# Optimization experiments

Measured on AMD Instinct MI355X. Metric: run time of the kernel, lower is better.

Reference implementation:

```python
import jax, jax.numpy as jnp
import numpy as np

EMBED_DIM = 384


def setup_inputs() -> dict:
    key = jax.random.key(0)
    k1, k2, k3 = jax.random.split(key, 3)
    B, P, N, C = 32, 4, 1024, EMBED_DIM
    x = jax.random.normal(k1, (B, P, N, C), dtype=jnp.float32)
    # 1x1 Conv2D on channel-last == linear on last dim; kernel [Cin, Cout]
    w_qkv = jax.random.normal(k2, (C, 1 + 2 * C), dtype=jnp.float32) * (1.0 / np.sqrt(C))
    b_qkv = jnp.zeros((1 + 2 * C,), dtype=jnp.float32)
    w_proj = jax.random.normal(k3, (C, C), dtype=jnp.float32) * (1.0 / np.sqrt(C))
    b_proj = jnp.zeros((C,), dtype=jnp.float32)
    return {"x": x, "w_qkv": w_qkv, "b_qkv": b_qkv, "w_proj": w_proj, "b_proj": b_proj}


def reference(x, w_qkv, b_qkv, w_proj, b_proj):
    C = EMBED_DIM
    # qkv pointwise conv: [B,P,N,C] @ [C, 1+2C]
    qkv = jnp.einsum('bpnc,cd->bpnd', x, w_qkv) + b_qkv
    query = qkv[..., :1]                 # [B,P,N,1]
    key_t = qkv[..., 1:1 + C]            # [B,P,N,C]
    value = qkv[..., 1 + C:]             # [B,P,N,C]
    # NOTE: softmax over the trailing axis of size 1 (faithful to source) -> all ones
    context_scores = jax.nn.softmax(query, axis=-1)
    # key * scores, reduce-sum over patch-index axis (axis=2), keepdims
    context_vector = jnp.sum(key_t * context_scores, axis=2, keepdims=True)  # [B,P,1,C]
    gated = jax.nn.relu(value) * context_vector                              # [B,P,N,C]
    out = jnp.einsum('bpnc,cd->bpnd', gated, w_proj) + b_proj
    return out
```

## Files before the change

kernel.cpp:

```cpp
#include <hip/hip_runtime.h>
#include <hip/hip_bf16.h>
#include <type_traits>
#include <utility>

#define C_    384
#define N_    1024
#define G_    128
#define QKVD  769

typedef float  f32x4 __attribute__((ext_vector_type(4)));
typedef short  s16x8 __attribute__((ext_vector_type(8)));
typedef __bf16 b16x8 __attribute__((ext_vector_type(8)));

template <typename V, typename = void>
struct mfma_takes : std::false_type {};
template <typename V>
struct mfma_takes<V, std::void_t<decltype(__builtin_amdgcn_mfma_f32_16x16x32_bf16(
    std::declval<V>(), std::declval<V>(), std::declval<f32x4>(), 0, 0, 0))>>
    : std::true_type {};

using frag_t = std::conditional_t<mfma_takes<s16x8>::value, s16x8, b16x8>;

template <typename V>
__device__ __forceinline__ f32x4 mfma_bf16(V a, V b, f32x4 c) {
  return __builtin_amdgcn_mfma_f32_16x16x32_bf16(a, b, c, 0, 0, 0);
}

__device__ __forceinline__ unsigned short f2bf(float f) {
  union { float f; unsigned u; } v; v.f = f;
  unsigned r = v.u + 0x7fffu + ((v.u >> 16) & 1u);
  return (unsigned short)(r >> 16);
}
__device__ __forceinline__ unsigned pack2(float lo, float hi) {
  return (unsigned)f2bf(lo) | ((unsigned)f2bf(hi) << 16);
}

__global__ __launch_bounds__(384) void k_xsum(const float* __restrict__ x,
                                              float* __restrict__ xsum) {
  __shared__ float sh[4][C_];
  const int tid = threadIdx.x;
  const int c4  = (tid % 96) * 4;
  const int rg  = tid / 96;
  const int b   = blockIdx.x;
  const int g   = b >> 3;
  const float* p = x + ((size_t)b * 128 + (size_t)rg * 32) * C_ + c4;
  f32x4 s = {0.f, 0.f, 0.f, 0.f};
#pragma unroll 8
  for (int r = 0; r < 32; ++r) {
    float4 v = *(const float4*)(p + (size_t)r * C_);
    s.x += v.x; s.y += v.y; s.z += v.z; s.w += v.w;
  }
  *(f32x4*)&sh[rg][c4] = s;
  __syncthreads();
  if (rg == 0) {
#pragma unroll
    for (int j = 0; j < 4; ++j) {
      float v = sh[0][c4 + j] + sh[1][c4 + j] + sh[2][c4 + j] + sh[3][c4 + j];
      atomicAdd(&xsum[g * C_ + c4 + j], v);
    }
  }
}

__global__ void k_cv(const float* __restrict__ xsum, const float* __restrict__ w_qkv,
                     const float* __restrict__ b_qkv, float* __restrict__ cv) {
  __shared__ float xs[C_];
  int g = blockIdx.x, c = threadIdx.x;
  xs[c] = xsum[g * C_ + c];
  __syncthreads();
  float acc = 0.f;
#pragma unroll 4
  for (int k = 0; k < C_; ++k) acc += xs[k] * w_qkv[k * QKVD + 1 + c];
  cv[g * C_ + c] = acc + (float)N_ * b_qkv[1 + c];
}

__global__ void k_pack(const float* __restrict__ w_qkv, const float* __restrict__ w_proj,
                       unsigned short* __restrict__ pWv, unsigned short* __restrict__ pWp) {
  int bid = blockIdx.x;
  int mat = bid / 288;
  int r   = bid % 288;
  int kk = r / 24, nf = r % 24;
  int lane = threadIdx.x;
  int kbase = kk * 32 + (lane >> 4) * 8;
  int n = nf * 16 + (lane & 15);
  unsigned v[4];
#pragma unroll
  for (int jj = 0; jj < 4; ++jj) {
    int k0 = kbase + jj * 2;
    float f0 = mat ? w_proj[(size_t)k0 * C_ + n]       : w_qkv[(size_t)k0 * QKVD + 385 + n];
    float f1 = mat ? w_proj[(size_t)(k0 + 1) * C_ + n] : w_qkv[(size_t)(k0 + 1) * QKVD + 385 + n];
    v[jj] = (unsigned)f2bf(f0) | ((unsigned)f2bf(f1) << 16);
  }
  unsigned short* dst = (mat ? pWp : pWv) + ((size_t)r * 64 + lane) * 8;
  uint4 w; w.x = v[0]; w.y = v[1]; w.z = v[2]; w.w = v[3];
  *(uint4*)dst = w;
}

__global__ __launch_bounds__(512) void k_fused(
    const float* __restrict__ x, const unsigned short* __restrict__ pWv,
    const unsigned short* __restrict__ pWp, const float* __restrict__ cv,
    const float* __restrict__ b_qkv, const float* __restrict__ b_proj,
    float* __restrict__ out) {
  __shared__ __align__(16) char tile[32 * 768];
  __shared__ float cv_l[C_], bv_l[C_], bp_l[C_];

  const int tid  = threadIdx.x;
  const int lane = tid & 63;
  const int wv   = tid >> 6;
  const int R0   = blockIdx.x * 32;
  const int g    = R0 >> 10;

  if (tid < C_) {
    cv_l[tid] = cv[g * C_ + tid];
    bv_l[tid] = b_qkv[1 + C_ + tid];
    bp_l[tid] = b_proj[tid];
  }

  {
    const float* xg = x + (size_t)R0 * C_;
#pragma unroll
    for (int j = 0; j < 3; ++j) {
      int ch  = tid + j * 512;
      int row = ch / 48;
      int c8  = (ch % 48) * 8;
      const float4* s0 = (const float4*)(xg + (size_t)row * C_ + c8);
      float4 a = s0[0], b = s0[1];
      uint4 w;
      w.x = pack2(a.x, a.y); w.y = pack2(a.z, a.w);
      w.z = pack2(b.x, b.y); w.w = pack2(b.z, b.w);
      int byte = (row * 768 + c8 * 2) ^ ((row & 7) << 4);
      *(uint4*)(tile + byte) = w;
    }
  }
  __syncthreads();

  const f32x4 zero = {0.f, 0.f, 0.f, 0.f};
  f32x4 acc[2][3];
#pragma unroll
  for (int m = 0; m < 2; ++m)
#pragma unroll
    for (int n = 0; n < 3; ++n) acc[m][n] = zero;

  for (int kk = 0; kk < 12; ++kk) {
    frag_t A[2], Bv[3];
    int kb2 = (kk * 32 + (lane >> 4) * 8) * 2;
#pragma unroll
    for (int m = 0; m < 2; ++m) {
      int row = m * 16 + (lane & 15);
      A[m] = *(const frag_t*)(tile + ((row * 768 + kb2) ^ ((row & 7) << 4)));
    }
    const unsigned short* bp_ = pWv + ((size_t)(kk * 24 + wv * 3) * 64 + lane) * 8;
#pragma unroll
    for (int n = 0; n < 3; ++n) Bv[n] = *(const frag_t*)(bp_ + (size_t)n * 64 * 8);
#pragma unroll
    for (int m = 0; m < 2; ++m)
#pragma unroll
      for (int n = 0; n < 3; ++n) acc[m][n] = mfma_bf16(A[m], Bv[n], acc[m][n]);
  }
  __syncthreads();

#pragma unroll
  for (int m = 0; m < 2; ++m) {
#pragma unroll
    for (int n = 0; n < 3; ++n) {
      int col = wv * 48 + n * 16 + (lane & 15);
      float cvv = cv_l[col], bvv = bv_l[col];
#pragma unroll
      for (int r = 0; r < 4; ++r) {
        int row = m * 16 + (lane >> 4) * 4 + r;
        float val = fmaxf(acc[m][n][r] + bvv, 0.f) * cvv;
        *(unsigned short*)(tile + ((row * 768 + col * 2) ^ ((row & 7) << 4))) = f2bf(val);
      }
    }
  }
  __syncthreads();

#pragma unroll
  for (int m = 0; m < 2; ++m)
#pragma unroll
    for (int n = 0; n < 3; ++n) acc[m][n] = zero;

  for (int kk = 0; kk < 12; ++kk) {
    frag_t A[2], Bv[3];
    int kb2 = (kk * 32 + (lane >> 4) * 8) * 2;
#pragma unroll
    for (int m = 0; m < 2; ++m) {
      int row = m * 16 + (lane & 15);
      A[m] = *(const frag_t*)(tile + ((row * 768 + kb2) ^ ((row & 7) << 4)));
    }
    const unsigned short* bp_ = pWp + ((size_t)(kk * 24 + wv * 3) * 64 + lane) * 8;
#pragma unroll
    for (int n = 0; n < 3; ++n) Bv[n] = *(const frag_t*)(bp_ + (size_t)n * 64 * 8);
#pragma unroll
    for (int m = 0; m < 2; ++m)
#pragma unroll
      for (int n = 0; n < 3; ++n) acc[m][n] = mfma_bf16(A[m], Bv[n], acc[m][n]);
  }

#pragma unroll
  for (int m = 0; m < 2; ++m) {
#pragma unroll
    for (int n = 0; n < 3; ++n) {
      int col = wv * 48 + n * 16 + (lane & 15);
      float bpv = bp_l[col];
#pragma unroll
      for (int r = 0; r < 4; ++r) {
        int row = m * 16 + (lane >> 4) * 4 + r;
        out[(size_t)(R0 + row) * C_ + col] = acc[m][n][r] + bpv;
      }
    }
  }
}

extern "C" void kernel_launch(void* const* d_in, const int* in_sizes, int n_in,
                              void* d_out, int out_size, void* d_ws, size_t ws_size,
                              hipStream_t stream) {
  const float* x      = (const float*)d_in[0];
  const float* w_qkv  = (const float*)d_in[1];
  const float* b_qkv  = (const float*)d_in[2];
  const float* w_proj = (const float*)d_in[3];
  const float* b_proj = (const float*)d_in[4];
  float* out = (float*)d_out;

  float* xsum = (float*)d_ws;
  float* cvp  = xsum + G_ * C_;
  unsigned short* pWv = (unsigned short*)(cvp + G_ * C_);
  unsigned short* pWp = pWv + C_ * C_;

  hipMemsetAsync(xsum, 0, G_ * C_ * sizeof(float), stream);
  k_xsum<<<1024, 384, 0, stream>>>(x, xsum);
  k_pack<<<576, 64, 0, stream>>>(w_qkv, w_proj, pWv, pWp);
  k_cv<<<G_, C_, 0, stream>>>(xsum, w_qkv, b_qkv, cvp);
  k_fused<<<4096, 512, 0, stream>>>(x, pWv, pWp, cvp, b_qkv, b_proj, out);
}
```

Before: 234.3 us.

## Pre-convert x to swizzled bf16 tiles while summing, stage via global_load_lds

A new prep kernel reads x once, computes the per-group column sums, and writes a bf16 copy of x already laid out in the swizzled LDS tile format into workspace. The fused kernel then copies each tile straight into LDS with global_load_lds instead of reading fp32 x and converting it, so the second full fp32 read of x becomes a half-size bf16 read. The cost is an extra write and read of the bf16 image in global memory. The new path runs only when the workspace is large enough; otherwise the old path is kept.

```diff
diff --git a/kernel.cpp b/kernel.cpp
--- a/kernel.cpp
+++ b/kernel.cpp
@@ -3,10 +3,11 @@
 #include <type_traits>
 #include <utility>
 
-#define C_    384
-#define N_    1024
-#define G_    128
-#define QKVD  769
+#define C_     384
+#define N_     1024
+#define G_     128
+#define QKVD   769
+#define TILE_B 24576
 
 typedef float  f32x4 __attribute__((ext_vector_type(4)));
 typedef short  s16x8 __attribute__((ext_vector_type(8)));
@@ -33,6 +34,53 @@
 }
 __device__ __forceinline__ unsigned pack2(float lo, float hi) {
   return (unsigned)f2bf(lo) | ((unsigned)f2bf(hi) << 16);
+}
+
+__device__ __forceinline__ void stage16(const char* g, char* lbase, int lane) {
+#if __has_builtin(__builtin_amdgcn_global_load_lds)
+  __builtin_amdgcn_global_load_lds(
+      (const __attribute__((address_space(1))) void*)g,
+      (__attribute__((address_space(3))) void*)lbase, 16, 0, 0);
+#else
+  *(uint4*)(lbase + lane * 16) = *(const uint4*)g;
+#endif
+}
+
+__global__ __launch_bounds__(384) void k_prep(const float* __restrict__ x,
+                                              char* __restrict__ xbb,
+                                              float* __restrict__ xsum) {
+  __shared__ float csum[C_];
+  const int b    = blockIdx.x;
+  const int g    = b >> 4;
+  const int tid  = threadIdx.x;
+  const int col8 = (tid % 48) * 8;
+  const int rg   = tid / 48;
+  csum[tid] = 0.f;
+  __syncthreads();
+
+  const float* xg = x + ((size_t)b * 64 + (size_t)rg * 8) * C_ + col8;
+  char* img = xbb + (size_t)b * 2 * TILE_B;
+  float s0=0,s1=0,s2=0,s3=0,s4=0,s5=0,s6=0,s7=0;
+#pragma unroll
+  for (int j = 0; j < 8; ++j) {
+    int row = rg * 8 + j;
+    float4 a = *(const float4*)(xg + (size_t)j * C_);
+    float4 c = *(const float4*)(xg + (size_t)j * C_ + 4);
+    uint4 w;
+    w.x = pack2(a.x, a.y); w.y = pack2(a.z, a.w);
+    w.z = pack2(c.x, c.y); w.w = pack2(c.z, c.w);
+    int rt = row & 31;
+    int tl = row >> 5;
+    *(uint4*)(img + tl * TILE_B + ((rt * 768 + col8 * 2) ^ ((rt & 7) << 4))) = w;
+    s0 += a.x; s1 += a.y; s2 += a.z; s3 += a.w;
+    s4 += c.x; s5 += c.y; s6 += c.z; s7 += c.w;
+  }
+  atomicAdd(&csum[col8 + 0], s0); atomicAdd(&csum[col8 + 1], s1);
+  atomicAdd(&csum[col8 + 2], s2); atomicAdd(&csum[col8 + 3], s3);
+  atomicAdd(&csum[col8 + 4], s4); atomicAdd(&csum[col8 + 5], s5);
+  atomicAdd(&csum[col8 + 6], s6); atomicAdd(&csum[col8 + 7], s7);
+  __syncthreads();
+  atomicAdd(&xsum[g * C_ + tid], csum[tid]);
 }
 
 __global__ __launch_bounds__(384) void k_xsum(const float* __restrict__ x,
@@ -95,11 +143,12 @@
   *(uint4*)dst = w;
 }
 
+template <bool PRE>
 __global__ __launch_bounds__(512) void k_fused(
-    const float* __restrict__ x, const unsigned short* __restrict__ pWv,
-    const unsigned short* __restrict__ pWp, const float* __restrict__ cv,
-    const float* __restrict__ b_qkv, const float* __restrict__ b_proj,
-    float* __restrict__ out) {
+    const float* __restrict__ x, const char* __restrict__ xbb,
+    const unsigned short* __restrict__ pWv, const unsigned short* __restrict__ pWp,
+    const float* __restrict__ cv, const float* __restrict__ b_qkv,
+    const float* __restrict__ b_proj, float* __restrict__ out) {
   __shared__ __align__(16) char tile[32 * 768];
   __shared__ float cv_l[C_], bv_l[C_], bp_l[C_];
 
@@ -115,7 +164,14 @@
     bp_l[tid] = b_proj[tid];
   }
 
-  {
+  if constexpr (PRE) {
+    const char* img = xbb + (size_t)blockIdx.x * TILE_B;
+#pragma unroll
+    for (int j = 0; j < 3; ++j) {
+      int cb = (wv * 3 + j) * 1024;
+      stage16(img + cb + lane * 16, tile + cb, lane);
+    }
+  } else {
     const float* xg = x + (size_t)R0 * C_;
 #pragma unroll
     for (int j = 0; j < 3; ++j) {
@@ -225,10 +281,20 @@
   float* cvp  = xsum + G_ * C_;
   unsigned short* pWv = (unsigned short*)(cvp + G_ * C_);
   unsigned short* pWp = pWv + C_ * C_;
+  char* xbb = (char*)(pWp + C_ * C_);
+
+  const size_t need = 983040 + (size_t)4096 * TILE_B;
 
   hipMemsetAsync(xsum, 0, G_ * C_ * sizeof(float), stream);
-  k_xsum<<<1024, 384, 0, stream>>>(x, xsum);
   k_pack<<<576, 64, 0, stream>>>(w_qkv, w_proj, pWv, pWp);
-  k_cv<<<G_, C_, 0, stream>>>(xsum, w_qkv, b_qkv, cvp);
-  k_fused<<<4096, 512, 0, stream>>>(x, pWv, pWp, cvp, b_qkv, b_proj, out);
-}
+
+  if (ws_size >= need) {
+    k_prep<<<2048, 384, 0, stream>>>(x, xbb, xsum);
+    k_cv<<<G_, C_, 0, stream>>>(xsum, w_qkv, b_qkv, cvp);
+    k_fused<true><<<4096, 512, 0, stream>>>(x, xbb, pWv, pWp, cvp, b_qkv, b_proj, out);
+  } else {
+    k_xsum<<<1024, 384, 0, stream>>>(x, xsum);
+    k_cv<<<G_, C_, 0, stream>>>(xsum, w_qkv, b_qkv, cvp);
+    k_fused<false><<<4096, 512, 0, stream>>>(x, xbb, pWv, pWp, cvp, b_qkv, b_proj, out);
+  }
+}
```

After: 233.1 us. About the same (-0.5%).
